# Kernel tuning notes

Hardware: AMD Instinct MI355X
Metric: run time of the kernel (lower is better)

## Reference

```python
import jax, jax.numpy as jnp
import numpy as np

E = 8      # num_experts
R = 32     # LoRA rank
D = 1024   # in_features (d_model)
H = 4096   # out_features of fc1 (hidden)
B = 2
S = 2048
SCALING = 1.0 / R  # lora_alpha / rank with alpha=1


def setup_inputs() -> dict:
    key = jax.random.key(0)
    ks = jax.random.split(key, 9)
    def w(k, shape, scale=0.02):
        return jax.random.normal(k, shape, dtype=jnp.float32) * scale
    return {
        "x": jax.random.normal(ks[0], (B, S, D), dtype=jnp.float32),
        "router_w": w(ks[1], (E, D)),
        "router_b": jnp.zeros((E,), jnp.float32),
        "fc1_w": w(ks[2], (H, D)),
        "fc1_b": jnp.zeros((H,), jnp.float32),
        "fc2_w": w(ks[3], (D, H)),
        "fc2_b": jnp.zeros((D,), jnp.float32),
        "A_down": w(ks[4], (E, R, D)),
        "Ab_down": jnp.zeros((E, R), jnp.float32),
        "B_down": w(ks[5], (E, H, R)),
        "Bb_down": jnp.zeros((E, H), jnp.float32),
        "A_up": w(ks[6], (E, R, H)),
        "Ab_up": jnp.zeros((E, R), jnp.float32),
        "B_up": w(ks[7], (E, D, R)),
        "Bb_up": jnp.zeros((E, D), jnp.float32),
    }


def _moe_lora(x, mask, A, Ab, Bw, Bb):
    # x: [B,S,din]; mask: one-hot [B,S,E]; A: [E,R,din]; Bw: [E,dout,R]
    # rank-stage for all experts is cheap (R=32), select per token via one-hot
    h = jnp.einsum('bsd,erd->bser', x, A) + Ab          # [B,S,E,R]
    hsel = jnp.einsum('bser,bse->bsr', h, mask)          # [B,S,R]
    out = jnp.zeros(x.shape[:2] + (Bw.shape[1],), dtype=x.dtype)
    for e in range(E):  # fixed small expert count; avoids [B,S,E,dout] blowup
        out = out + mask[..., e:e + 1] * (hsel @ Bw[e].T + Bb[e])
    return out * SCALING


def reference(x, router_w, router_b, fc1_w, fc1_b, fc2_w, fc2_b,
              A_down, Ab_down, B_down, Bb_down,
              A_up, Ab_up, B_up, Bb_up):
    logits = x @ router_w.T + router_b                   # [B,S,E]
    routing = jax.nn.softmax(logits, axis=-1)
    index = jnp.argmax(logits, axis=-1)                  # top-1 expert [B,S]
    mask = jax.nn.one_hot(index, E, dtype=x.dtype)       # y_hard [B,S,E]
    expert_choice = mask - jax.lax.stop_gradient(routing) + routing
    # down: frozen fc1 + sparse LoRA (dropout layers in eval mode -> identity)
    down = x @ fc1_w.T + fc1_b + _moe_lora(x, mask, A_down, Ab_down, B_down, Bb_down)
    a = jax.nn.gelu(down, approximate=False)             # F.gelu exact
    up = a @ fc2_w.T + fc2_b + _moe_lora(a, mask, A_up, Ab_up, B_up, Bb_up)
    return up, routing, expert_choice
```

## Files before the change

kernel.cpp:

```cpp
#include <hip/hip_runtime.h>
#include <hip/hip_bf16.h>
#include <math.h>
#include <stdint.h>

#define E_ 8
#define R_ 32
#define D_ 1024
#define H_ 4096
#define NTOK 4096
#define M_MAX 5120
#define TILES_MAX 40
#define SCALING 0.03125f

typedef __attribute__((ext_vector_type(8))) __bf16 bf16x8;
typedef __attribute__((ext_vector_type(8))) unsigned short ushort8;
typedef __attribute__((ext_vector_type(4))) float floatx4;

__device__ __forceinline__ unsigned short f2b(float f) {
    union { float f; unsigned int i; } v; v.f = f;
    unsigned int x = v.i;
    x += 0x7fffu + ((x >> 16) & 1u);
    return (unsigned short)(x >> 16);
}
__device__ __forceinline__ float gelu_fast(float v) {
    float u = v * (0.7978845608028654f + 0.0356774080857f * v * v);
    float t = __expf(-2.f * fabsf(u));
    float th = (1.f - t) * __builtin_amdgcn_rcpf(1.f + t);
    th = (u >= 0.f) ? th : -th;
    return 0.5f * v * (1.f + th);
}

#define GLOAD_LDS16(g, l) __builtin_amdgcn_global_load_lds( \
    (const __attribute__((address_space(1))) void*)(g),     \
    (__attribute__((address_space(3))) void*)(l), 16, 0, 0)

__global__ __launch_bounds__(256) void k_prep(
    const float* __restrict__ w1, const float* __restrict__ w2,
    const float* __restrict__ Ad, const float* __restrict__ Bd,
    const float* __restrict__ Au, const float* __restrict__ Bu,
    unsigned short* __restrict__ w1b, unsigned short* __restrict__ w2b,
    unsigned short* __restrict__ Adb, unsigned short* __restrict__ Bdb,
    unsigned short* __restrict__ Aub, unsigned short* __restrict__ Bub,
    const float* __restrict__ x, const float* __restrict__ rw,
    const float* __restrict__ rb,
    float* __restrict__ out, int* __restrict__ idx)
{
    if (blockIdx.x < 5376) {
        long g = ((long)blockIdx.x * 256 + threadIdx.x) * 8;
        const float* src; unsigned short* dst; long off;
        if      (g <  4194304L) { src = w1; dst = w1b; off = 0; }
        else if (g <  8388608L) { src = w2; dst = w2b; off = 4194304L; }
        else if (g <  8650752L) { src = Ad; dst = Adb; off = 8388608L; }
        else if (g <  9699328L) { src = Bd; dst = Bdb; off = 8650752L; }
        else if (g < 10747904L) { src = Au; dst = Aub; off = 9699328L; }
        else                    { src = Bu; dst = Bub; off = 10747904L; }
        long i = g - off;
        float4 a = *(const float4*)(src + i);
        float4 b = *(const float4*)(src + i + 4);
        ushort8 o;
        o[0] = f2b(a.x); o[1] = f2b(a.y); o[2] = f2b(a.z); o[3] = f2b(a.w);
        o[4] = f2b(b.x); o[5] = f2b(b.y); o[6] = f2b(b.z); o[7] = f2b(b.w);
        *(ushort8*)(dst + i) = o;
        return;
    }
    const int wave = threadIdx.x >> 6, lane = threadIdx.x & 63;
    const int t = (blockIdx.x - 5376) * 4 + wave;
    const float4* xr = (const float4*)(x + (size_t)t * D_);
    float4 xv[4];
#pragma unroll
    for (int s = 0; s < 4; ++s) xv[s] = xr[lane + 64 * s];
    float acc[E_];
#pragma unroll
    for (int e = 0; e < E_; ++e) {
        const float4* wr = (const float4*)(rw + (size_t)e * D_);
        float s = 0.f;
#pragma unroll
        for (int u = 0; u < 4; ++u) {
            float4 wv = wr[lane + 64 * u];
            s += xv[u].x * wv.x + xv[u].y * wv.y + xv[u].z * wv.z + xv[u].w * wv.w;
        }
        acc[e] = s;
    }
#pragma unroll
    for (int e = 0; e < E_; ++e) {
#pragma unroll
        for (int m = 32; m > 0; m >>= 1) acc[e] += __shfl_xor(acc[e], m, 64);
        acc[e] += rb[e];
    }
    int best = 0;
#pragma unroll
    for (int e = 1; e < E_; ++e) if (acc[e] > acc[best]) best = e;
    const float mx = acc[best];
    float pr[E_]; float se = 0.f;
#pragma unroll
    for (int e = 0; e < E_; ++e) { pr[e] = expf(acc[e] - mx); se += pr[e]; }
    const float inv = 1.f / se;
    if (lane < E_) {
        float r = pr[lane] * inv;
        out[(size_t)NTOK * D_ + (size_t)t * E_ + lane] = r;
        float maskv = (lane == best) ? 1.f : 0.f;
        out[(size_t)NTOK * D_ + (size_t)NTOK * E_ + (size_t)t * E_ + lane] = (maskv - r) + r;
    }
    if (lane == 0) idx[t] = best;
}

__global__ __launch_bounds__(256) void k_scan(
    const int* __restrict__ idx, int* __restrict__ hdr,
    int* __restrict__ tile_e, int* __restrict__ gather)
{
    __shared__ int cnt[256][E_];
    __shared__ int tot[E_], base[E_];
    const int tid = threadIdx.x;
    for (int m = tid; m < M_MAX; m += 256) gather[m] = -1;
    int c[E_];
#pragma unroll
    for (int e = 0; e < E_; ++e) c[e] = 0;
    for (int t = tid * 16; t < tid * 16 + 16; ++t) c[idx[t] & 7]++;
#pragma unroll
    for (int e = 0; e < E_; ++e) cnt[tid][e] = c[e];
    __syncthreads();
    if (tid < E_) {
        int run = 0;
        for (int i = 0; i < 256; ++i) { int v = cnt[i][tid]; cnt[i][tid] = run; run += v; }
        tot[tid] = run;
    }
    __syncthreads();
    if (tid == 0) {
        int b = 0, tp = 0;
        for (int e = 0; e < E_; ++e) {
            base[e] = b;
            int nt = (tot[e] + 127) >> 7;
            for (int k = 0; k < nt; ++k) tile_e[tp++] = e;
            b += nt << 7;
        }
        hdr[0] = b;
        hdr[1] = tp;
        for (int k = tp; k < TILES_MAX; ++k) tile_e[k] = 0;
    }
    __syncthreads();
    int p[E_];
#pragma unroll
    for (int e = 0; e < E_; ++e) p[e] = base[e] + cnt[tid][e];
    for (int t = tid * 16; t < tid * 16 + 16; ++t) { int e = idx[t] & 7; gather[p[e]++] = t; }
}

__global__ __launch_bounds__(128) void k_gather(
    const float* __restrict__ x, const int* __restrict__ gather,
    unsigned short* __restrict__ xg)
{
    const int m = blockIdx.x, tid = threadIdx.x;
    const int t = gather[m];
    ushort8* dst = (ushort8*)(xg + (size_t)m * D_);
    ushort8 o;
    if ((unsigned)t < (unsigned)NTOK) {
        const float4* src = (const float4*)(x + (size_t)t * D_);
        float4 a = src[tid * 2], b = src[tid * 2 + 1];
        o[0] = f2b(a.x); o[1] = f2b(a.y); o[2] = f2b(a.z); o[3] = f2b(a.w);
        o[4] = f2b(b.x); o[5] = f2b(b.y); o[6] = f2b(b.z); o[7] = f2b(b.w);
    } else {
        o = (ushort8)(0);
    }
    dst[tid] = o;
}

__global__ __launch_bounds__(256) void k_lora_a2(
    const unsigned short* __restrict__ A,
    const unsigned short* __restrict__ W,
    const float* __restrict__ Ab,
    const int* __restrict__ hdr, const int* __restrict__ tile_e,
    unsigned short* __restrict__ outb,
    int Ktot)
{
    const int mtile = blockIdx.y;
    int ntiles = hdr[1]; if (ntiles > TILES_MAX) ntiles = TILES_MAX;
    if (mtile >= ntiles) return;
    const int e = tile_e[mtile] & 7;
    const int m0 = mtile * 128 + blockIdx.x * 32;
    const int wave = threadIdx.x >> 6, lane = threadIdx.x & 63;
    const int q = lane >> 4, l16 = lane & 15;
    const int Ks = Ktot >> 2;
    const int kbase = wave * Ks;
    const floatx4 z4 = {0.f, 0.f, 0.f, 0.f};
    floatx4 acc[2][2] = {{z4, z4}, {z4, z4}};
    const bf16x8* A0 = (const bf16x8*)(A + (size_t)(m0 + l16) * Ktot);
    const bf16x8* A1 = (const bf16x8*)(A + (size_t)(m0 + 16 + l16) * Ktot);
    const bf16x8* W0 = (const bf16x8*)(W + ((size_t)e * 32 + l16) * Ktot);
    const bf16x8* W1 = (const bf16x8*)(W + ((size_t)e * 32 + 16 + l16) * Ktot);
    for (int k = kbase; k < kbase + Ks; k += 32) {
        int u = (k >> 3) + q;
        bf16x8 a0 = A0[u], a1 = A1[u];
        bf16x8 b0 = W0[u], b1 = W1[u];
        acc[0][0] = __builtin_amdgcn_mfma_f32_16x16x32_bf16(a0, b0, acc[0][0], 0, 0, 0);
        acc[0][1] = __builtin_amdgcn_mfma_f32_16x16x32_bf16(a0, b1, acc[0][1], 0, 0, 0);
        acc[1][0] = __builtin_amdgcn_mfma_f32_16x16x32_bf16(a1, b0, acc[1][0], 0, 0, 0);
        acc[1][1] = __builtin_amdgcn_mfma_f32_16x16x32_bf16(a1, b1, acc[1][1], 0, 0, 0);
    }
    __shared__ float red[4][32][32];
#pragma unroll
    for (int mi = 0; mi < 2; ++mi)
#pragma unroll
        for (int ni = 0; ni < 2; ++ni)
#pragma unroll
            for (int r = 0; r < 4; ++r)
                red[wave][mi * 16 + q * 4 + r][ni * 16 + l16] = acc[mi][ni][r];
    __syncthreads();
    for (int i = threadIdx.x; i < 1024; i += 256) {
        int lr = i >> 5, c = i & 31;
        float s = red[0][lr][c] + red[1][lr][c] + red[2][lr][c] + red[3][lr][c];
        outb[(size_t)(m0 + lr) * 32 + c] = f2b(SCALING * (s + Ab[e * 32 + c]));
    }
}

template <int KTOT, bool IS_FC1, int NSPLIT>
__global__ __launch_bounds__(256) void k_mlp(
    const unsigned short* __restrict__ Amat,
    const unsigned short* __restrict__ Wmat,
    const float* __restrict__ bias,
    const unsigned short* __restrict__ lora_h,
    const unsigned short* __restrict__ lora_B,
    const float* __restrict__ lora_b,
    const int* __restrict__ hdr, const int* __restrict__ tile_e,
    const int* __restrict__ gather,
    unsigned short* __restrict__ outb,
    float* __restrict__ outf,
    float* __restrict__ P,
    int NOUT)
{
    const int mtile = blockIdx.y;
    int ntiles = hdr[1]; if (ntiles > TILES_MAX) ntiles = TILES_MAX;
    if (mtile >= ntiles) return;
    const int e = tile_e[mtile] & 7;
    const int h0 = blockIdx.x * 128;
    const int m0 = mtile * 128;
    const bool extras = (NSPLIT == 1) || (blockIdx.z == 0);
    const int Kslice = KTOT / NSPLIT;
    const int kstart = blockIdx.z * Kslice;
    __shared__ bf16x8 As[1024];
    __shared__ bf16x8 Bs[1024];
    const int tid = threadIdx.x;
    const int lane = tid & 63;
    const int q = lane >> 4, l16 = lane & 15;
    const int wave = tid >> 6;
    const int wm = wave & 1, wn = wave >> 1;
    const floatx4 z4 = {0.f, 0.f, 0.f, 0.f};
    floatx4 acc[4][4];
#pragma unroll
    for (int mi = 0; mi < 4; ++mi)
#pragma unroll
        for (int ni = 0; ni < 4; ++ni) acc[mi][ni] = z4;

    const unsigned short* Abase = Amat + (size_t)m0 * KTOT;
    const unsigned short* Bbase = Wmat + (size_t)h0 * KTOT;

    for (int k0 = kstart; k0 < kstart + Kslice; k0 += 64) {
#pragma unroll
        for (int rnd = 0; rnd < 4; ++rnd) {
            int s = rnd * 256 + tid;
            int row = s >> 3;
            int jj = (s & 7) ^ (row & 7);
            const unsigned short* ga = Abase + (size_t)row * KTOT + k0 + jj * 8;
            const unsigned short* gb = Bbase + (size_t)row * KTOT + k0 + jj * 8;
            GLOAD_LDS16(ga, As + rnd * 256 + wave * 64);
            GLOAD_LDS16(gb, Bs + rnd * 256 + wave * 64);
        }
        __syncthreads();
#pragma unroll
        for (int ka = 0; ka < 2; ++ka) {
            bf16x8 af[4], bfr[4];
#pragma unroll
            for (int mi = 0; mi < 4; ++mi) {
                int row = wm * 64 + mi * 16 + l16;
                af[mi] = As[row * 8 + ((ka * 4 + q) ^ (row & 7))];
            }
#pragma unroll
            for (int ni = 0; ni < 4; ++ni) {
                int row = wn * 64 + ni * 16 + l16;
                bfr[ni] = Bs[row * 8 + ((ka * 4 + q) ^ (row & 7))];
            }
#pragma unroll
            for (int mi = 0; mi < 4; ++mi)
#pragma unroll
                for (int ni = 0; ni < 4; ++ni)
                    acc[mi][ni] = __builtin_amdgcn_mfma_f32_16x16x32_bf16(af[mi], bfr[ni], acc[mi][ni], 0, 0, 0);
        }
        __syncthreads();
    }

    if (extras) {
        bf16x8 a2[4], b2[4];
#pragma unroll
        for (int mi = 0; mi < 4; ++mi)
            a2[mi] = *(const bf16x8*)(lora_h + (size_t)(m0 + wm * 64 + mi * 16 + l16) * 32 + q * 8);
#pragma unroll
        for (int ni = 0; ni < 4; ++ni)
            b2[ni] = *(const bf16x8*)(lora_B + ((size_t)e * NOUT + h0 + wn * 64 + ni * 16 + l16) * 32 + q * 8);
#pragma unroll
        for (int mi = 0; mi < 4; ++mi)
#pragma unroll
            for (int ni = 0; ni < 4; ++ni)
                acc[mi][ni] = __builtin_amdgcn_mfma_f32_16x16x32_bf16(a2[mi], b2[ni], acc[mi][ni], 0, 0, 0);
    }

#pragma unroll
    for (int ni = 0; ni < 4; ++ni) {
        int gh = h0 + wn * 64 + ni * 16 + l16;
        float bv = extras ? (bias[gh] + SCALING * lora_b[e * NOUT + gh]) : 0.f;
#pragma unroll
        for (int mi = 0; mi < 4; ++mi) {
#pragma unroll
            for (int r = 0; r < 4; ++r) {
                int gm = m0 + wm * 64 + mi * 16 + q * 4 + r;
                float v = acc[mi][ni][r] + bv;
                if (IS_FC1) {
                    outb[(size_t)gm * NOUT + gh] = f2b(gelu_fast(v));
                } else if (extras) {
                    int t = gather[gm];
                    if ((unsigned)t < (unsigned)NTOK) outf[(size_t)t * NOUT + gh] = v;
                } else {
                    P[(size_t)gm * NOUT + gh] = v;
                }
            }
        }
    }
}

__global__ __launch_bounds__(256) void k_reduce(
    const float* __restrict__ P, const int* __restrict__ gather,
    float* __restrict__ out)
{
    const int m = blockIdx.x;
    const int t = gather[m];
    if ((unsigned)t >= (unsigned)NTOK) return;
    const float4* p4 = (const float4*)(P + (size_t)m * D_);
    float4* o4 = (float4*)(out + (size_t)t * D_);
    int i = threadIdx.x;
    float4 a = o4[i], b = p4[i];
    a.x += b.x; a.y += b.y; a.z += b.z; a.w += b.w;
    o4[i] = a;
}

#define OFF_IDX      0u
#define OFF_HDR      16384u
#define OFF_TILE     16640u
#define OFF_GATHER   16896u
#define OFF_XG       37376u
#define OFF_W1B      10523136u
#define OFF_ADB      18911744u
#define OFF_BDB      19436032u
#define OFF_HSB      21533184u
#define OFF_P        37376u
#define OFF_AG       21860864u
#define OFF_HUB      63803904u
#define OFF_W2B      64131584u
#define OFF_AUB      72520192u
#define OFF_BUB      74617344u
#define WS_NEEDED    75141632u

extern "C" void kernel_launch(void* const* d_in, const int* in_sizes, int n_in,
                              void* d_out, int out_size, void* d_ws, size_t ws_size,
                              hipStream_t stream)
{
    (void)out_size;
    if (ws_size < (size_t)WS_NEEDED) return;
    if (n_in < 15 || in_sizes[0] != NTOK * D_ || in_sizes[3] != H_ * D_ ||
        in_sizes[5] != D_ * H_ || in_sizes[9] != E_ * H_ * R_) return;

    const float* x   = (const float*)d_in[0];
    const float* rw  = (const float*)d_in[1];
    const float* rb  = (const float*)d_in[2];
    const float* w1  = (const float*)d_in[3];
    const float* b1  = (const float*)d_in[4];
    const float* w2  = (const float*)d_in[5];
    const float* b2  = (const float*)d_in[6];
    const float* Ad  = (const float*)d_in[7];
    const float* Abd = (const float*)d_in[8];
    const float* Bd  = (const float*)d_in[9];
    const float* Bbd = (const float*)d_in[10];
    const float* Au  = (const float*)d_in[11];
    const float* Abu = (const float*)d_in[12];
    const float* Bu  = (const float*)d_in[13];
    const float* Bbu = (const float*)d_in[14];
    float* out = (float*)d_out;
    char* ws = (char*)d_ws;

    int* idx            = (int*)(ws + OFF_IDX);
    int* hdr            = (int*)(ws + OFF_HDR);
    int* tile_e         = (int*)(ws + OFF_TILE);
    int* gather         = (int*)(ws + OFF_GATHER);
    unsigned short* xg  = (unsigned short*)(ws + OFF_XG);
    unsigned short* hsb = (unsigned short*)(ws + OFF_HSB);
    unsigned short* ag  = (unsigned short*)(ws + OFF_AG);
    unsigned short* hub = (unsigned short*)(ws + OFF_HUB);
    unsigned short* w1b = (unsigned short*)(ws + OFF_W1B);
    unsigned short* w2b = (unsigned short*)(ws + OFF_W2B);
    unsigned short* Adb = (unsigned short*)(ws + OFF_ADB);
    unsigned short* Bdb = (unsigned short*)(ws + OFF_BDB);
    unsigned short* Aub = (unsigned short*)(ws + OFF_AUB);
    unsigned short* Bub = (unsigned short*)(ws + OFF_BUB);
    float* P            = (float*)(ws + OFF_P);

    k_prep<<<6400, 256, 0, stream>>>(w1, w2, Ad, Bd, Au, Bu,
                                     w1b, w2b, Adb, Bdb, Aub, Bub,
                                     x, rw, rb, out, idx);
    k_scan<<<1, 256, 0, stream>>>(idx, hdr, tile_e, gather);
    k_gather<<<M_MAX, 128, 0, stream>>>(x, gather, xg);
    k_lora_a2<<<dim3(4, TILES_MAX), 256, 0, stream>>>(xg, Adb, Abd, hdr, tile_e, hsb, D_);
    k_mlp<D_, true, 1><<<dim3(H_ / 128, TILES_MAX, 1), 256, 0, stream>>>(
        xg, w1b, b1, hsb, Bdb, Bbd, hdr, tile_e, gather, ag, nullptr, nullptr, H_);
    k_lora_a2<<<dim3(4, TILES_MAX), 256, 0, stream>>>(ag, Aub, Abu, hdr, tile_e, hub, H_);
    k_mlp<H_, false, 2><<<dim3(D_ / 128, TILES_MAX, 2), 256, 0, stream>>>(
        ag, w2b, b2, hub, Bub, Bbu, hdr, tile_e, gather, nullptr, out, P, D_);
    k_reduce<<<M_MAX, 256, 0, stream>>>(P, gather, out);
}
```

Measured before the change: 306.7 us.

## Fuse down-LoRA A projection into gather and replace fc2 split-K with narrower tiles

The gather kernel now also computes the down-projection LoRA rank-32 activations per token with scalar fp32 dot products, which removes the separate k_lora_a2 launch for fc1. The fc2 GEMM drops its two-way split-K plus reduce kernel and instead uses 64-wide N tiles, giving the same block count without a partial buffer or an extra pass. The cost is that the fused LoRA-A work runs on scalar ALUs rather than MFMA, and fc2 blocks now each run the full K=4096 loop at lower per-block arithmetic intensity.

```diff
diff --git a/kernel.cpp b/kernel.cpp
--- a/kernel.cpp
+++ b/kernel.cpp
@@ -16,6 +16,9 @@
 typedef __attribute__((ext_vector_type(8))) unsigned short ushort8;
 typedef __attribute__((ext_vector_type(4))) float floatx4;
 
+__device__ __forceinline__ float b2f(unsigned short u) {
+    union { unsigned int i; float f; } v; v.i = ((unsigned int)u) << 16; return v.f;
+}
 __device__ __forceinline__ unsigned short f2b(float f) {
     union { float f; unsigned int i; } v; v.f = f;
     unsigned int x = v.i;
@@ -145,22 +148,48 @@
 }
 
 __global__ __launch_bounds__(128) void k_gather(
-    const float* __restrict__ x, const int* __restrict__ gather,
-    unsigned short* __restrict__ xg)
+    const float* __restrict__ x, const unsigned short* __restrict__ Adb,
+    const float* __restrict__ Abd,
+    const int* __restrict__ gather, const int* __restrict__ tile_e,
+    unsigned short* __restrict__ xg, unsigned short* __restrict__ hsb)
 {
     const int m = blockIdx.x, tid = threadIdx.x;
     const int t = gather[m];
-    ushort8* dst = (ushort8*)(xg + (size_t)m * D_);
-    ushort8 o;
-    if ((unsigned)t < (unsigned)NTOK) {
-        const float4* src = (const float4*)(x + (size_t)t * D_);
-        float4 a = src[tid * 2], b = src[tid * 2 + 1];
-        o[0] = f2b(a.x); o[1] = f2b(a.y); o[2] = f2b(a.z); o[3] = f2b(a.w);
-        o[4] = f2b(b.x); o[5] = f2b(b.y); o[6] = f2b(b.z); o[7] = f2b(b.w);
-    } else {
-        o = (ushort8)(0);
-    }
-    dst[tid] = o;
+    const int e = tile_e[m >> 7] & 7;
+    const bool valid = (unsigned)t < (unsigned)NTOK;
+    {
+        ushort8* dst = (ushort8*)(xg + (size_t)m * D_);
+        ushort8 o;
+        if (valid) {
+            const float4* src = (const float4*)(x + (size_t)t * D_);
+            float4 a = src[tid * 2], b = src[tid * 2 + 1];
+            o[0] = f2b(a.x); o[1] = f2b(a.y); o[2] = f2b(a.z); o[3] = f2b(a.w);
+            o[4] = f2b(b.x); o[5] = f2b(b.y); o[6] = f2b(b.z); o[7] = f2b(b.w);
+        } else {
+            o = (ushort8)(0);
+        }
+        dst[tid] = o;
+    }
+    const int r = tid & 31, c = tid >> 5;
+    float s = 0.f;
+    if (valid) {
+        const float4* xv = (const float4*)(x + (size_t)t * D_ + c * 256);
+        const ushort8* av = (const ushort8*)(Adb + ((size_t)e * 32 + r) * D_ + c * 256);
+#pragma unroll 4
+        for (int i = 0; i < 32; ++i) {
+            float4 xa = xv[i * 2], xb = xv[i * 2 + 1];
+            ushort8 a8 = av[i];
+            s += xa.x * b2f(a8[0]) + xa.y * b2f(a8[1]) + xa.z * b2f(a8[2]) + xa.w * b2f(a8[3])
+               + xb.x * b2f(a8[4]) + xb.y * b2f(a8[5]) + xb.z * b2f(a8[6]) + xb.w * b2f(a8[7]);
+        }
+    }
+    __shared__ float part[32][4];
+    part[r][c] = s;
+    __syncthreads();
+    if (tid < 32) {
+        float ss = part[tid][0] + part[tid][1] + part[tid][2] + part[tid][3];
+        hsb[(size_t)m * 32 + tid] = f2b(SCALING * (ss + Abd[e * 32 + tid]));
+    }
 }
 
 __global__ __launch_bounds__(256) void k_lora_a2(
@@ -211,7 +240,7 @@
     }
 }
 
-template <int KTOT, bool IS_FC1, int NSPLIT>
+template <int KTOT, int BN, bool IS_FC1>
 __global__ __launch_bounds__(256) void k_mlp(
     const unsigned short* __restrict__ Amat,
     const unsigned short* __restrict__ Wmat,
@@ -223,88 +252,89 @@
     const int* __restrict__ gather,
     unsigned short* __restrict__ outb,
     float* __restrict__ outf,
-    float* __restrict__ P,
     int NOUT)
 {
+    constexpr int NI = BN / 32;
     const int mtile = blockIdx.y;
     int ntiles = hdr[1]; if (ntiles > TILES_MAX) ntiles = TILES_MAX;
     if (mtile >= ntiles) return;
     const int e = tile_e[mtile] & 7;
-    const int h0 = blockIdx.x * 128;
+    const int h0 = blockIdx.x * BN;
     const int m0 = mtile * 128;
-    const bool extras = (NSPLIT == 1) || (blockIdx.z == 0);
-    const int Kslice = KTOT / NSPLIT;
-    const int kstart = blockIdx.z * Kslice;
     __shared__ bf16x8 As[1024];
-    __shared__ bf16x8 Bs[1024];
+    __shared__ bf16x8 Bs[BN * 8];
     const int tid = threadIdx.x;
     const int lane = tid & 63;
     const int q = lane >> 4, l16 = lane & 15;
     const int wave = tid >> 6;
     const int wm = wave & 1, wn = wave >> 1;
     const floatx4 z4 = {0.f, 0.f, 0.f, 0.f};
-    floatx4 acc[4][4];
+    floatx4 acc[4][NI];
 #pragma unroll
     for (int mi = 0; mi < 4; ++mi)
 #pragma unroll
-        for (int ni = 0; ni < 4; ++ni) acc[mi][ni] = z4;
+        for (int ni = 0; ni < NI; ++ni) acc[mi][ni] = z4;
 
     const unsigned short* Abase = Amat + (size_t)m0 * KTOT;
     const unsigned short* Bbase = Wmat + (size_t)h0 * KTOT;
 
-    for (int k0 = kstart; k0 < kstart + Kslice; k0 += 64) {
+    for (int k0 = 0; k0 < KTOT; k0 += 64) {
 #pragma unroll
         for (int rnd = 0; rnd < 4; ++rnd) {
             int s = rnd * 256 + tid;
             int row = s >> 3;
             int jj = (s & 7) ^ (row & 7);
-            const unsigned short* ga = Abase + (size_t)row * KTOT + k0 + jj * 8;
-            const unsigned short* gb = Bbase + (size_t)row * KTOT + k0 + jj * 8;
-            GLOAD_LDS16(ga, As + rnd * 256 + wave * 64);
-            GLOAD_LDS16(gb, Bs + rnd * 256 + wave * 64);
+            GLOAD_LDS16(Abase + (size_t)row * KTOT + k0 + jj * 8, As + rnd * 256 + wave * 64);
+        }
+#pragma unroll
+        for (int rnd = 0; rnd < BN / 32; ++rnd) {
+            int s = rnd * 256 + tid;
+            int row = s >> 3;
+            int jj = (s & 7) ^ (row & 7);
+            GLOAD_LDS16(Bbase + (size_t)row * KTOT + k0 + jj * 8, Bs + rnd * 256 + wave * 64);
         }
         __syncthreads();
 #pragma unroll
         for (int ka = 0; ka < 2; ++ka) {
-            bf16x8 af[4], bfr[4];
+            bf16x8 af[4], bfr[NI];
 #pragma unroll
             for (int mi = 0; mi < 4; ++mi) {
                 int row = wm * 64 + mi * 16 + l16;
                 af[mi] = As[row * 8 + ((ka * 4 + q) ^ (row & 7))];
             }
 #pragma unroll
-            for (int ni = 0; ni < 4; ++ni) {
-                int row = wn * 64 + ni * 16 + l16;
+            for (int ni = 0; ni < NI; ++ni) {
+                int row = wn * (BN / 2) + ni * 16 + l16;
                 bfr[ni] = Bs[row * 8 + ((ka * 4 + q) ^ (row & 7))];
             }
 #pragma unroll
             for (int mi = 0; mi < 4; ++mi)
 #pragma unroll
-                for (int ni = 0; ni < 4; ++ni)
+                for (int ni = 0; ni < NI; ++ni)
                     acc[mi][ni] = __builtin_amdgcn_mfma_f32_16x16x32_bf16(af[mi], bfr[ni], acc[mi][ni], 0, 0, 0);
         }
         __syncthreads();
     }
 
-    if (extras) {
-        bf16x8 a2[4], b2[4];
+    {
+        bf16x8 a2[4], b2[NI];
 #pragma unroll
         for (int mi = 0; mi < 4; ++mi)
             a2[mi] = *(const bf16x8*)(lora_h + (size_t)(m0 + wm * 64 + mi * 16 + l16) * 32 + q * 8);
 #pragma unroll
-        for (int ni = 0; ni < 4; ++ni)
-            b2[ni] = *(const bf16x8*)(lora_B + ((size_t)e * NOUT + h0 + wn * 64 + ni * 16 + l16) * 32 + q * 8);
+        for (int ni = 0; ni < NI; ++ni)
+            b2[ni] = *(const bf16x8*)(lora_B + ((size_t)e * NOUT + h0 + wn * (BN / 2) + ni * 16 + l16) * 32 + q * 8);
 #pragma unroll
         for (int mi = 0; mi < 4; ++mi)
 #pragma unroll
-            for (int ni = 0; ni < 4; ++ni)
+            for (int ni = 0; ni < NI; ++ni)
                 acc[mi][ni] = __builtin_amdgcn_mfma_f32_16x16x32_bf16(a2[mi], b2[ni], acc[mi][ni], 0, 0, 0);
     }
 
 #pragma unroll
-    for (int ni = 0; ni < 4; ++ni) {
-        int gh = h0 + wn * 64 + ni * 16 + l16;
-        float bv = extras ? (bias[gh] + SCALING * lora_b[e * NOUT + gh]) : 0.f;
+    for (int ni = 0; ni < NI; ++ni) {
+        int gh = h0 + wn * (BN / 2) + ni * 16 + l16;
+        float bv = bias[gh] + SCALING * lora_b[e * NOUT + gh];
 #pragma unroll
         for (int mi = 0; mi < 4; ++mi) {
 #pragma unroll
@@ -313,30 +343,13 @@
                 float v = acc[mi][ni][r] + bv;
                 if (IS_FC1) {
                     outb[(size_t)gm * NOUT + gh] = f2b(gelu_fast(v));
-                } else if (extras) {
+                } else {
                     int t = gather[gm];
                     if ((unsigned)t < (unsigned)NTOK) outf[(size_t)t * NOUT + gh] = v;
-                } else {
-                    P[(size_t)gm * NOUT + gh] = v;
                 }
             }
         }
     }
-}
-
-__global__ __launch_bounds__(256) void k_reduce(
-    const float* __restrict__ P, const int* __restrict__ gather,
-    float* __restrict__ out)
-{
-    const int m = blockIdx.x;
-    const int t = gather[m];
-    if ((unsigned)t >= (unsigned)NTOK) return;
-    const float4* p4 = (const float4*)(P + (size_t)m * D_);
-    float4* o4 = (float4*)(out + (size_t)t * D_);
-    int i = threadIdx.x;
-    float4 a = o4[i], b = p4[i];
-    a.x += b.x; a.y += b.y; a.z += b.z; a.w += b.w;
-    o4[i] = a;
 }
 
 #define OFF_IDX      0u
@@ -348,7 +361,6 @@
 #define OFF_ADB      18911744u
 #define OFF_BDB      19436032u
 #define OFF_HSB      21533184u
-#define OFF_P        37376u
 #define OFF_AG       21860864u
 #define OFF_HUB      63803904u
 #define OFF_W2B      64131584u
@@ -397,18 +409,15 @@
     unsigned short* Bdb = (unsigned short*)(ws + OFF_BDB);
     unsigned short* Aub = (unsigned short*)(ws + OFF_AUB);
     unsigned short* Bub = (unsigned short*)(ws + OFF_BUB);
-    float* P            = (float*)(ws + OFF_P);
 
     k_prep<<<6400, 256, 0, stream>>>(w1, w2, Ad, Bd, Au, Bu,
                                      w1b, w2b, Adb, Bdb, Aub, Bub,
                                      x, rw, rb, out, idx);
     k_scan<<<1, 256, 0, stream>>>(idx, hdr, tile_e, gather);
-    k_gather<<<M_MAX, 128, 0, stream>>>(x, gather, xg);
-    k_lora_a2<<<dim3(4, TILES_MAX), 256, 0, stream>>>(xg, Adb, Abd, hdr, tile_e, hsb, D_);
-    k_mlp<D_, true, 1><<<dim3(H_ / 128, TILES_MAX, 1), 256, 0, stream>>>(
-        xg, w1b, b1, hsb, Bdb, Bbd, hdr, tile_e, gather, ag, nullptr, nullptr, H_);
+    k_gather<<<M_MAX, 128, 0, stream>>>(x, Adb, Abd, gather, tile_e, xg, hsb);
+    k_mlp<D_, 128, true><<<dim3(H_ / 128, TILES_MAX), 256, 0, stream>>>(
+        xg, w1b, b1, hsb, Bdb, Bbd, hdr, tile_e, gather, ag, nullptr, H_);
     k_lora_a2<<<dim3(4, TILES_MAX), 256, 0, stream>>>(ag, Aub, Abu, hdr, tile_e, hub, H_);
-    k_mlp<H_, false, 2><<<dim3(D_ / 128, TILES_MAX, 2), 256, 0, stream>>>(
-        ag, w2b, b2, hub, Bub, Bbu, hdr, tile_e, gather, nullptr, out, P, D_);
-    k_reduce<<<M_MAX, 256, 0, stream>>>(P, gather, out);
-}
+    k_mlp<H_, 64, false><<<dim3(D_ / 64, TILES_MAX), 256, 0, stream>>>(
+        ag, w2b, b2, hub, Bub, Bbu, hdr, tile_e, gather, nullptr, out, D_);
+}
```

New measurement: 340.2 us. 1.11x slower.
